# Kernel tuning notes

Measured on AMD Instinct MI355X. Metric: run time of the kernel, lower is better.

The kernel has to match this reference:

```python
import jax, jax.numpy as jnp
import numpy as np

DIM = 1024
HEADS = 16
HEAD_DIM = DIM // HEADS
EPS = 1e-5


def layer_norm(x, w, b):
    # normalize over last dim (head_dim)
    mu = jnp.mean(x, axis=-1, keepdims=True)
    var = jnp.mean(jnp.square(x - mu), axis=-1, keepdims=True)
    return (x - mu) * jax.lax.rsqrt(var + EPS) * w + b


def setup_inputs() -> dict:
    key = jax.random.key(0)
    ks = jax.random.split(key, 8)
    B, N = 2, 2048
    x = jax.random.normal(ks[0], (B, N, DIM), dtype=jnp.float32)
    mask = jax.random.randint(ks[1], (B, 1, N, N), 0, 2) == 1  # True = masked out
    qkv_w = jax.random.normal(ks[2], (3 * DIM, DIM), dtype=jnp.float32) * (DIM ** -0.5)
    q_norm_w = jnp.ones((HEAD_DIM,), dtype=jnp.float32)
    q_norm_b = jnp.zeros((HEAD_DIM,), dtype=jnp.float32)
    k_norm_w = jnp.ones((HEAD_DIM,), dtype=jnp.float32)
    k_norm_b = jnp.zeros((HEAD_DIM,), dtype=jnp.float32)
    proj_w = jax.random.normal(ks[3], (DIM, DIM), dtype=jnp.float32) * (DIM ** -0.5)
    proj_b = jnp.zeros((DIM,), dtype=jnp.float32)
    return {"x": x, "mask": mask, "qkv_w": qkv_w,
            "q_norm_w": q_norm_w, "q_norm_b": q_norm_b,
            "k_norm_w": k_norm_w, "k_norm_b": k_norm_b,
            "proj_w": proj_w, "proj_b": proj_b}


def reference(x, mask, qkv_w, q_norm_w, q_norm_b, k_norm_w, k_norm_b, proj_w, proj_b):
    B, N, C = x.shape
    H, D = HEADS, HEAD_DIM
    scale = D ** -0.5
    # qkv projection (no bias), split into q,k,v of shape (B,H,N,D)
    qkv = (x @ qkv_w.T).reshape(B, N, 3, H, D).transpose(2, 0, 3, 1, 4)
    q, k, v = qkv[0], qkv[1], qkv[2]
    q = layer_norm(q, q_norm_w, q_norm_b)
    k = layer_norm(k, k_norm_w, k_norm_b)
    q = q * scale
    attn = jnp.einsum("bhnd,bhmd->bhnm", q, k)  # (B,H,N,N)
    attn = jnp.where(mask, -jnp.inf, attn)
    attn = jax.nn.softmax(attn, axis=-1)
    out = jnp.einsum("bhnm,bhmd->bhnd", attn, v)
    out = out.transpose(0, 2, 1, 3).reshape(B, N, C)
    return out @ proj_w.T + proj_b
```

## Files before the change

### kernel.cpp

```cpp
#include <hip/hip_runtime.h>
#include <hip/hip_bf16.h>
#include <math.h>

#define B_    2
#define N_    2048
#define DIM_  1024
#define H_    16
#define HD_   64
#define EPS_  1e-5f
#define SCALE_ 0.125f
#define LOG2E_ 1.4426950408889634f
#define MFIX_  14.0f

typedef __attribute__((ext_vector_type(8))) __bf16 bf16x8;
typedef __attribute__((ext_vector_type(8))) unsigned short ushort8;
typedef __attribute__((ext_vector_type(4))) float f32x4;

__device__ __forceinline__ unsigned short f2bf(float x) {
    unsigned u = __builtin_bit_cast(unsigned, x);
    u += 0x7fff + ((u >> 16) & 1);
    return (unsigned short)(u >> 16);
}
__device__ __forceinline__ unsigned pk2bf(float a, float b) {
    unsigned ua = __builtin_bit_cast(unsigned, a) + 0x8000u;
    unsigned ub = __builtin_bit_cast(unsigned, b) + 0x8000u;
    return __builtin_amdgcn_perm(ub, ua, 0x07060302);
}

__device__ __forceinline__ void gl_lds16(const void* g, void* l) {
    __builtin_amdgcn_global_load_lds(
        (const __attribute__((address_space(1))) void*)g,
        (__attribute__((address_space(3))) void*)l, 16, 0, 0);
}

__global__ __launch_bounds__(256) void cast_all_bf16(
    const float* __restrict__ x, const float* __restrict__ qkvw,
    const float* __restrict__ pw, unsigned short* __restrict__ out) {
    int i = (blockIdx.x * 256 + threadIdx.x) * 8;
    const float* src;
    if (i < 4194304) src = x + i;
    else if (i < 7340032) src = qkvw + (i - 4194304);
    else src = pw + (i - 7340032);
    float4 v0 = *(const float4*)src;
    float4 v1 = *(const float4*)(src + 4);
    ushort8 r;
    r[0] = f2bf(v0.x); r[1] = f2bf(v0.y); r[2] = f2bf(v0.z); r[3] = f2bf(v0.w);
    r[4] = f2bf(v1.x); r[5] = f2bf(v1.y); r[6] = f2bf(v1.z); r[7] = f2bf(v1.w);
    *(ushort8*)(out + i) = r;
}

__global__ __launch_bounds__(256) void pack_mask(
    const int* __restrict__ mask, unsigned long long* __restrict__ bm) {
    int w = blockIdx.x * 4 + (threadIdx.x >> 6);
    int lane = threadIdx.x & 63;
    int mv = mask[(size_t)w * 64 + lane];
    unsigned long long bits = __ballot(mv != 0);
    if (lane == 0) bm[w] = bits;
}

__global__ __launch_bounds__(256) void gemm_qkv_ln(
    const unsigned short* __restrict__ A, const unsigned short* __restrict__ Bw,
    const float* __restrict__ qnw, const float* __restrict__ qnb,
    const float* __restrict__ knw, const float* __restrict__ knb,
    unsigned short* __restrict__ qbuf, unsigned short* __restrict__ kbuf,
    unsigned short* __restrict__ vbuf) {
    const int K = DIM_;
    __shared__ unsigned short As[128 * 32];
    __shared__ unsigned short Bs[128 * 32];
    const int tid = threadIdx.x;
    const int wave = tid >> 6, lane = tid & 63;
    const int quad = lane >> 4, lcol = lane & 15;
    const int wr = wave >> 1, wc = wave & 1;
    const int row0 = blockIdx.y * 128, col0 = blockIdx.x * 128;

    f32x4 acc[4][4];
#pragma unroll
    for (int i = 0; i < 4; ++i)
#pragma unroll
        for (int j = 0; j < 4; ++j) acc[i][j] = (f32x4){0.f, 0.f, 0.f, 0.f};

    for (int k0 = 0; k0 < K; k0 += 32) {
        __syncthreads();
#pragma unroll
        for (int c = 0; c < 2; ++c) {
            int base = wave * 2048 + c * 1024;
            int myofs = base + lane * 16;
            int r = myofs >> 6;
            int kb = myofs & 63;
            gl_lds16((const char*)A + ((size_t)(row0 + r) * K + k0) * 2 + kb,
                     (char*)As + base);
            gl_lds16((const char*)Bw + ((size_t)(col0 + r) * K + k0) * 2 + kb,
                     (char*)Bs + base);
        }
        __syncthreads();

        bf16x8 af[4], bfr[4];
#pragma unroll
        for (int i = 0; i < 4; ++i) {
            af[i] = *(const bf16x8*)&As[(wr * 64 + i * 16 + lcol) * 32 + quad * 8];
            bfr[i] = *(const bf16x8*)&Bs[(wc * 64 + i * 16 + lcol) * 32 + quad * 8];
        }
#pragma unroll
        for (int i = 0; i < 4; ++i)
#pragma unroll
            for (int j = 0; j < 4; ++j)
                acc[i][j] = __builtin_amdgcn_mfma_f32_16x16x32_bf16(
                    af[i], bfr[j], acc[i][j], 0, 0, 0);
    }

    const int colbase = col0 + wc * 64;
    const int t = colbase >> 10;
    const int h = (colbase & 1023) >> 6;

    if (t < 2) {
        const float* wv = (t == 0) ? qnw : knw;
        const float* bv = (t == 0) ? qnb : knb;
        float wreg[4], breg[4];
#pragma unroll
        for (int j = 0; j < 4; ++j) {
            wreg[j] = wv[j * 16 + lcol];
            breg[j] = bv[j * 16 + lcol];
        }
        const float sc = (t == 0) ? (SCALE_ * LOG2E_) : 1.f;
        unsigned short* obase = (t == 0) ? qbuf : kbuf;
#pragma unroll
        for (int i = 0; i < 4; ++i) {
#pragma unroll
            for (int reg = 0; reg < 4; ++reg) {
                int row = row0 + wr * 64 + i * 16 + quad * 4 + reg;
                int bb = row >> 11, n = row & (N_ - 1);
                float v[4];
#pragma unroll
                for (int j = 0; j < 4; ++j) v[j] = acc[i][j][reg];
                float s = v[0] + v[1] + v[2] + v[3];
                s += __shfl_xor(s, 1);
                s += __shfl_xor(s, 2);
                s += __shfl_xor(s, 4);
                s += __shfl_xor(s, 8);
                float mu = s * (1.f / 64.f);
                float d[4], s2 = 0.f;
#pragma unroll
                for (int j = 0; j < 4; ++j) {
                    d[j] = v[j] - mu;
                    s2 += d[j] * d[j];
                }
                s2 += __shfl_xor(s2, 1);
                s2 += __shfl_xor(s2, 2);
                s2 += __shfl_xor(s2, 4);
                s2 += __shfl_xor(s2, 8);
                float r = rsqrtf(s2 * (1.f / 64.f) + EPS_);
                unsigned short* dst =
                    obase + ((size_t)(bb * H_ + h) * N_ + n) * 64 + lcol;
#pragma unroll
                for (int j = 0; j < 4; ++j)
                    dst[j * 16] = f2bf((d[j] * r * wreg[j] + breg[j]) * sc);
            }
        }
    } else {
        const int dcol = colbase & 1023;
#pragma unroll
        for (int i = 0; i < 4; ++i) {
#pragma unroll
            for (int reg = 0; reg < 4; ++reg) {
                int row = row0 + wr * 64 + i * 16 + quad * 4 + reg;
                unsigned short* dst = vbuf + (size_t)row * DIM_ + dcol + lcol;
#pragma unroll
                for (int j = 0; j < 4; ++j)
                    dst[j * 16] = f2bf(acc[i][j][reg]);
            }
        }
    }
}

template <int WITH_BIAS, int OUT_BF16>
__global__ __launch_bounds__(256) void gemm_bt_mfma(
    const unsigned short* __restrict__ A, const unsigned short* __restrict__ Bw,
    const float* __restrict__ bias, void* __restrict__ Cout, int M, int Ncols,
    int K) {
    __shared__ unsigned short As[128 * 32];
    __shared__ unsigned short Bs[128 * 32];
    const int tid = threadIdx.x;
    const int wave = tid >> 6, lane = tid & 63;
    const int quad = lane >> 4, lcol = lane & 15;
    const int wr = wave >> 1, wc = wave & 1;
    const int row0 = blockIdx.y * 128, col0 = blockIdx.x * 128;

    f32x4 acc[4][4];
#pragma unroll
    for (int i = 0; i < 4; ++i)
#pragma unroll
        for (int j = 0; j < 4; ++j) acc[i][j] = (f32x4){0.f, 0.f, 0.f, 0.f};

    for (int k0 = 0; k0 < K; k0 += 32) {
        __syncthreads();
#pragma unroll
        for (int c = 0; c < 2; ++c) {
            int base = wave * 2048 + c * 1024;
            int myofs = base + lane * 16;
            int r = myofs >> 6;
            int kb = myofs & 63;
            gl_lds16((const char*)A + ((size_t)(row0 + r) * K + k0) * 2 + kb,
                     (char*)As + base);
            gl_lds16((const char*)Bw + ((size_t)(col0 + r) * K + k0) * 2 + kb,
                     (char*)Bs + base);
        }
        __syncthreads();

        bf16x8 af[4], bfr[4];
#pragma unroll
        for (int i = 0; i < 4; ++i) {
            af[i] = *(const bf16x8*)&As[(wr * 64 + i * 16 + lcol) * 32 + quad * 8];
            bfr[i] = *(const bf16x8*)&Bs[(wc * 64 + i * 16 + lcol) * 32 + quad * 8];
        }
#pragma unroll
        for (int i = 0; i < 4; ++i)
#pragma unroll
            for (int j = 0; j < 4; ++j)
                acc[i][j] = __builtin_amdgcn_mfma_f32_16x16x32_bf16(
                    af[i], bfr[j], acc[i][j], 0, 0, 0);
    }

#pragma unroll
    for (int i = 0; i < 4; ++i) {
#pragma unroll
        for (int j = 0; j < 4; ++j) {
            int col = col0 + wc * 64 + j * 16 + lcol;
            float bv = WITH_BIAS ? bias[col] : 0.f;
#pragma unroll
            for (int reg = 0; reg < 4; ++reg) {
                int row = row0 + wr * 64 + i * 16 + quad * 4 + reg;
                float v = acc[i][j][reg] + bv;
                if (OUT_BF16)
                    ((unsigned short*)Cout)[(size_t)row * Ncols + col] = f2bf(v);
                else
                    ((float*)Cout)[(size_t)row * Ncols + col] = v;
            }
        }
    }
}

__global__ __launch_bounds__(256) void transpose_v(
    const unsigned short* __restrict__ vbuf, unsigned short* __restrict__ vt) {
    __shared__ unsigned short Ts[64 * 65];
    const int tid = threadIdx.x;
    const int bh = blockIdx.y, n0 = blockIdx.x * 64;
    const int b = bh >> 4, h = bh & 15;
    {
        int r = tid >> 2, s = tid & 3;
        const unsigned short* src =
            vbuf + (size_t)(b * N_ + n0 + r) * DIM_ + h * 64 + s * 16;
#pragma unroll
        for (int i = 0; i < 16; ++i) Ts[r * 65 + s * 16 + i] = src[i];
    }
    __syncthreads();
    {
        int d = tid >> 2, ks = tid & 3;
        __align__(16) unsigned short tmp[16];
#pragma unroll
        for (int i = 0; i < 16; ++i) tmp[i] = Ts[(ks * 16 + i) * 65 + d];
        unsigned short* dst = vt + (size_t)(bh * 64 + d) * N_ + n0 + ks * 16;
        *(int4*)dst = *(const int4*)&tmp[0];
        *(int4*)(dst + 8) = *(const int4*)&tmp[8];
    }
}

__global__ __launch_bounds__(256) void flash_attn_mfma5(
    const unsigned short* __restrict__ q, const unsigned short* __restrict__ k,
    const unsigned short* __restrict__ vt,
    const unsigned long long* __restrict__ bm, unsigned short* __restrict__ ao) {
    __shared__ unsigned short Qs[64 * 64];
    __shared__ unsigned short Ks[2][64 * 64];
    __shared__ unsigned short Vts[2][64 * 64];
    __shared__ unsigned short Ps[4][16 * 72];

    const int tid = threadIdx.x;
    const int wave = tid >> 6, lane = tid & 63;
    const int quad = lane >> 4, lcol = lane & 15;
    const int bh = blockIdx.y, b = bh >> 4, h = bh & 15;
    const int q0 = blockIdx.x * 64;

    const char* kgbase = (const char*)k + (size_t)bh * N_ * 128;
    const char* vtbase = (const char*)vt + (size_t)bh * 64 * N_ * 2;

    const char* kp[2];
    const char* vp[2];
#pragma unroll
    for (int ci = 0; ci < 2; ++ci) {
        int c = wave * 2 + ci;
        int swz = (c & 3) * 2;
        kp[ci] = kgbase + (size_t)(lane ^ swz) * 128 + c * 16;
        vp[ci] = vtbase + ((size_t)(lane ^ swz) * N_ + c * 8) * 2;
    }

    {
        const char* qg = (const char*)(q + (size_t)(bh * N_ + q0) * 64);
#pragma unroll
        for (int c = 0; c < 2; ++c) {
            int base = wave * 2048 + c * 1024;
            gl_lds16(qg + base + lane * 16, (char*)Qs + base);
        }
#pragma unroll
        for (int ci = 0; ci < 2; ++ci) {
            int c = wave * 2 + ci;
            gl_lds16(kp[ci], (char*)Ks[0] + c * 1024);
            gl_lds16(vp[ci], (char*)Vts[0] + c * 1024);
            kp[ci] += 64 * 128;
            vp[ci] += 64 * 2;
        }
    }
    const unsigned long long* bmq =
        bm + ((size_t)b * N_ + q0 + wave * 16 + lcol) * 32;
    unsigned long long mw_next = bmq[0];
    __syncthreads();

    bf16x8 bq[2];
#pragma unroll
    for (int d0 = 0; d0 < 2; ++d0)
        bq[d0] = *(const bf16x8*)&Qs[(wave * 16 + lcol) * 64 + d0 * 32 + quad * 8];

    ushort8 ot;
#pragma unroll
    for (int i = 0; i < 8; ++i) ot[i] = 0x3F80;
    const bf16x8 ones = __builtin_bit_cast(bf16x8, ot);

    f32x4 oacc[4];
#pragma unroll
    for (int dt = 0; dt < 4; ++dt) oacc[dt] = (f32x4){0.f, 0.f, 0.f, 0.f};
    f32x4 lacc = (f32x4){0.f, 0.f, 0.f, 0.f};

    for (int k0 = 0; k0 < N_; k0 += 64) {
        const int cur = (k0 >> 6) & 1;
        const unsigned long long mw = mw_next;
        if (k0 + 64 < N_) {
#pragma unroll
            for (int ci = 0; ci < 2; ++ci) {
                int c = wave * 2 + ci;
                gl_lds16(kp[ci], (char*)Ks[cur ^ 1] + c * 1024);
                gl_lds16(vp[ci], (char*)Vts[cur ^ 1] + c * 1024);
                kp[ci] += 64 * 128;
                vp[ci] += 64 * 2;
            }
            mw_next = bmq[(k0 >> 6) + 1];
        }

        unsigned long long mq = mw >> (quad * 4);
        unsigned mlo = (unsigned)mq, mhi = (unsigned)(mq >> 32);
        f32x4 sacc[4];
#pragma unroll
        for (int kt = 0; kt < 4; ++kt) {
            unsigned word = (kt < 2) ? mlo : mhi;
            const int sh = (kt & 1) * 16;
#pragma unroll
            for (int reg = 0; reg < 4; ++reg)
                sacc[kt][reg] = ((word >> (sh + reg)) & 1u) ? -1e4f : -MFIX_;
        }

        const char* ksb = (const char*)Ks[cur];
        const char* vsb = (const char*)Vts[cur];
#pragma unroll
        for (int kt = 0; kt < 4; ++kt) {
#pragma unroll
            for (int d0 = 0; d0 < 2; ++d0) {
                int p = d0 * 4 + quad;
                bf16x8 ak = *(const bf16x8*)(ksb + p * 1024 +
                                             (((kt * 16 + lcol) ^ (quad * 2)) << 4));
                sacc[kt] = __builtin_amdgcn_mfma_f32_16x16x32_bf16(
                    ak, bq[d0], sacc[kt], 0, 0, 0);
            }
        }

#pragma unroll
        for (int kt = 0; kt < 4; ++kt) {
            float p0 = exp2f(sacc[kt][0]);
            float p1 = exp2f(sacc[kt][1]);
            float p2 = exp2f(sacc[kt][2]);
            float p3 = exp2f(sacc[kt][3]);
            uint2 pk;
            pk.x = pk2bf(p0, p1);
            pk.y = pk2bf(p2, p3);
            *(uint2*)&Ps[wave][lcol * 72 + kt * 16 + quad * 4] = pk;
        }

#pragma unroll
        for (int k2 = 0; k2 < 2; ++k2) {
            bf16x8 pf =
                *(const bf16x8*)&Ps[wave][lcol * 72 + k2 * 32 + quad * 8];
            lacc = __builtin_amdgcn_mfma_f32_16x16x32_bf16(ones, pf, lacc,
                                                           0, 0, 0);
#pragma unroll
            for (int dt = 0; dt < 4; ++dt) {
                int p = k2 * 4 + quad;
                bf16x8 vf = *(const bf16x8*)(vsb + p * 1024 +
                                             (((dt * 16 + lcol) ^ (quad * 2)) << 4));
                oacc[dt] = __builtin_amdgcn_mfma_f32_16x16x32_bf16(
                    vf, pf, oacc[dt], 0, 0, 0);
            }
        }
        __syncthreads();
    }

    float inv = 1.f / lacc[0];
    int row = q0 + wave * 16 + lcol;
    unsigned short* dst = ao + ((size_t)(b * N_ + row)) * DIM_ + h * 64 + quad * 4;
#pragma unroll
    for (int dt = 0; dt < 4; ++dt) {
        uint2 pk;
        pk.x = pk2bf(oacc[dt][0] * inv, oacc[dt][1] * inv);
        pk.y = pk2bf(oacc[dt][2] * inv, oacc[dt][3] * inv);
        *(uint2*)(dst + dt * 16) = pk;
    }
}

extern "C" void kernel_launch(void* const* d_in, const int* in_sizes, int n_in,
                              void* d_out, int out_size, void* d_ws,
                              size_t ws_size, hipStream_t stream) {
    const float* x     = (const float*)d_in[0];
    const int*   mask  = (const int*)d_in[1];
    const float* qkv_w = (const float*)d_in[2];
    const float* qnw   = (const float*)d_in[3];
    const float* qnb   = (const float*)d_in[4];
    const float* knw   = (const float*)d_in[5];
    const float* knb   = (const float*)d_in[6];
    const float* pw    = (const float*)d_in[7];
    const float* pb    = (const float*)d_in[8];
    float* out = (float*)d_out;

    char* ws = (char*)d_ws;
    unsigned short* x_bf  = (unsigned short*)(ws + 0);
    unsigned short* qw_bf = (unsigned short*)(ws + 8388608);
    unsigned short* pw_bf = (unsigned short*)(ws + 14680064);
    unsigned short* qbuf  = (unsigned short*)(ws + 16777216);
    unsigned short* kbuf  = (unsigned short*)(ws + 25165824);
    unsigned short* vbuf  = (unsigned short*)(ws + 33554432);
    unsigned short* vt    = (unsigned short*)(ws + 41943040);
    unsigned long long* bmask = (unsigned long long*)(ws + 50331648);
    unsigned short* ao_bnc = vbuf;

    cast_all_bf16<<<8388608 / 2048, 256, 0, stream>>>(x, qkv_w, pw, x_bf);

    gemm_qkv_ln<<<dim3(3072 / 128, 4096 / 128), 256, 0, stream>>>(
        x_bf, qw_bf, qnw, qnb, knw, knb, qbuf, kbuf, vbuf);

    transpose_v<<<dim3(N_ / 64, B_ * H_), 256, 0, stream>>>(vbuf, vt);

    pack_mask<<<(B_ * N_ * (N_ / 64)) / 4, 256, 0, stream>>>(mask, bmask);

    flash_attn_mfma5<<<dim3(N_ / 64, B_ * H_), 256, 0, stream>>>(
        qbuf, kbuf, vt, bmask, ao_bnc);

    gemm_bt_mfma<1, 0><<<dim3(DIM_ / 128, 4096 / 128), 256, 0, stream>>>(
        ao_bnc, pw_bf, pb, out, B_ * N_, DIM_, DIM_);
}
```

Before: 309.7 us.

## Keep softmax probabilities in registers by permuting V transpose layout

The V transpose now writes each 64-key chunk in a permuted key order. That order matches the register layout of the QK^T MFMA output. The attention kernel can then feed the packed bf16 probabilities directly as the B operand of the PV and row-sum MFMAs, with no round trip through a per-wave LDS scratch buffer. This removes LDS writes and reads and frees shared memory, at the cost of smaller 8-byte scattered global stores in the transpose kernel.

```diff
diff --git a/kernel.cpp b/kernel.cpp
--- a/kernel.cpp
+++ b/kernel.cpp
@@ -15,6 +15,7 @@
 typedef __attribute__((ext_vector_type(8))) __bf16 bf16x8;
 typedef __attribute__((ext_vector_type(8))) unsigned short ushort8;
 typedef __attribute__((ext_vector_type(4))) float f32x4;
+typedef __attribute__((ext_vector_type(4))) unsigned int uint4v;
 
 __device__ __forceinline__ unsigned short f2bf(float x) {
     unsigned u = __builtin_bit_cast(unsigned, x);
@@ -254,24 +255,27 @@
     }
     __syncthreads();
     {
-        int d = tid >> 2, ks = tid & 3;
-        __align__(16) unsigned short tmp[16];
-#pragma unroll
-        for (int i = 0; i < 16; ++i) tmp[i] = Ts[(ks * 16 + i) * 65 + d];
-        unsigned short* dst = vt + (size_t)(bh * 64 + d) * N_ + n0 + ks * 16;
-        *(int4*)dst = *(const int4*)&tmp[0];
-        *(int4*)(dst + 8) = *(const int4*)&tmp[8];
-    }
-}
-
-__global__ __launch_bounds__(256) void flash_attn_mfma5(
+        int d = tid >> 2, kt = tid & 3;
+        unsigned short* dstrow = vt + (size_t)(bh * 64 + d) * N_ + n0;
+        int P = kt >> 1, t = kt & 1;
+#pragma unroll
+        for (int q = 0; q < 4; ++q) {
+            __align__(8) unsigned short tmp4[4];
+#pragma unroll
+            for (int j = 0; j < 4; ++j)
+                tmp4[j] = Ts[(kt * 16 + q * 4 + j) * 65 + d];
+            *(uint2*)(dstrow + P * 32 + q * 8 + t * 4) = *(const uint2*)tmp4;
+        }
+    }
+}
+
+__global__ __launch_bounds__(256) void flash_attn_mfma6(
     const unsigned short* __restrict__ q, const unsigned short* __restrict__ k,
     const unsigned short* __restrict__ vt,
     const unsigned long long* __restrict__ bm, unsigned short* __restrict__ ao) {
     __shared__ unsigned short Qs[64 * 64];
     __shared__ unsigned short Ks[2][64 * 64];
     __shared__ unsigned short Vts[2][64 * 64];
-    __shared__ unsigned short Ps[4][16 * 72];
 
     const int tid = threadIdx.x;
     const int wave = tid >> 6, lane = tid & 63;
@@ -289,7 +293,7 @@
         int c = wave * 2 + ci;
         int swz = (c & 3) * 2;
         kp[ci] = kgbase + (size_t)(lane ^ swz) * 128 + c * 16;
-        vp[ci] = vtbase + ((size_t)(lane ^ swz) * N_ + c * 8) * 2;
+        vp[ci] = vtbase + (size_t)(lane ^ swz) * N_ * 2 + c * 16;
     }
 
     {
@@ -369,31 +373,34 @@
             }
         }
 
+        uint2 pk[4];
 #pragma unroll
         for (int kt = 0; kt < 4; ++kt) {
             float p0 = exp2f(sacc[kt][0]);
             float p1 = exp2f(sacc[kt][1]);
             float p2 = exp2f(sacc[kt][2]);
             float p3 = exp2f(sacc[kt][3]);
-            uint2 pk;
-            pk.x = pk2bf(p0, p1);
-            pk.y = pk2bf(p2, p3);
-            *(uint2*)&Ps[wave][lcol * 72 + kt * 16 + quad * 4] = pk;
-        }
-
-#pragma unroll
-        for (int k2 = 0; k2 < 2; ++k2) {
-            bf16x8 pf =
-                *(const bf16x8*)&Ps[wave][lcol * 72 + k2 * 32 + quad * 8];
-            lacc = __builtin_amdgcn_mfma_f32_16x16x32_bf16(ones, pf, lacc,
+            pk[kt].x = pk2bf(p0, p1);
+            pk[kt].y = pk2bf(p2, p3);
+        }
+
+#pragma unroll
+        for (int P = 0; P < 2; ++P) {
+            uint4v bu;
+            bu[0] = pk[2 * P].x;
+            bu[1] = pk[2 * P].y;
+            bu[2] = pk[2 * P + 1].x;
+            bu[3] = pk[2 * P + 1].y;
+            bf16x8 bp = __builtin_bit_cast(bf16x8, bu);
+            lacc = __builtin_amdgcn_mfma_f32_16x16x32_bf16(ones, bp, lacc,
                                                            0, 0, 0);
 #pragma unroll
             for (int dt = 0; dt < 4; ++dt) {
-                int p = k2 * 4 + quad;
-                bf16x8 vf = *(const bf16x8*)(vsb + p * 1024 +
+                int c = P * 4 + quad;
+                bf16x8 va = *(const bf16x8*)(vsb + c * 1024 +
                                              (((dt * 16 + lcol) ^ (quad * 2)) << 4));
                 oacc[dt] = __builtin_amdgcn_mfma_f32_16x16x32_bf16(
-                    vf, pf, oacc[dt], 0, 0, 0);
+                    va, bp, oacc[dt], 0, 0, 0);
             }
         }
         __syncthreads();
@@ -404,10 +411,10 @@
     unsigned short* dst = ao + ((size_t)(b * N_ + row)) * DIM_ + h * 64 + quad * 4;
 #pragma unroll
     for (int dt = 0; dt < 4; ++dt) {
-        uint2 pk;
-        pk.x = pk2bf(oacc[dt][0] * inv, oacc[dt][1] * inv);
-        pk.y = pk2bf(oacc[dt][2] * inv, oacc[dt][3] * inv);
-        *(uint2*)(dst + dt * 16) = pk;
+        uint2 pko;
+        pko.x = pk2bf(oacc[dt][0] * inv, oacc[dt][1] * inv);
+        pko.y = pk2bf(oacc[dt][2] * inv, oacc[dt][3] * inv);
+        *(uint2*)(dst + dt * 16) = pko;
     }
 }
 
@@ -445,7 +452,7 @@
 
     pack_mask<<<(B_ * N_ * (N_ / 64)) / 4, 256, 0, stream>>>(mask, bmask);
 
-    flash_attn_mfma5<<<dim3(N_ / 64, B_ * H_), 256, 0, stream>>>(
+    flash_attn_mfma6<<<dim3(N_ / 64, B_ * H_), 256, 0, stream>>>(
         qbuf, kbuf, vt, bmask, ao_bnc);
 
     gemm_bt_mfma<1, 0><<<dim3(DIM_ / 128, 4096 / 128), 256, 0, stream>>>(
```

New measurement: 293.5 us. 5.2% less time.
